# Kernel optimization log

Hardware: AMD Instinct MI355X
Metric: run time of the kernel (lower is better)

## Reference

```python
import jax, jax.numpy as jnp
import numpy as np

N_HEADS = 16
EMBED_DIM = 1024
HEAD_DIM = EMBED_DIM // N_HEADS
B, S = 4, 2048


def setup_inputs() -> dict:
    key = jax.random.key(0)
    k1, k2, k3, k4 = jax.random.split(key, 4)
    scale = 1.0 / np.sqrt(EMBED_DIM)
    x = jax.random.normal(k1, (B, S, EMBED_DIM), dtype=jnp.float32)
    Wq = jax.random.normal(k2, (EMBED_DIM, EMBED_DIM), dtype=jnp.float32) * scale
    Wk = jax.random.normal(k3, (EMBED_DIM, EMBED_DIM), dtype=jnp.float32) * scale
    Wv = jax.random.normal(k4, (EMBED_DIM, EMBED_DIM), dtype=jnp.float32) * scale
    return {"x": x, "Wq": Wq, "Wk": Wk, "Wv": Wv}


def reference(x, Wq, Wk, Wv):
    b, s, d = x.shape
    # torch nn.Linear(bias=False): y = x @ W.T
    def proj(W):
        return (x @ W.T).reshape(b, s, N_HEADS, HEAD_DIM).transpose(0, 2, 1, 3)  # [b,h,s,hd]
    q, k, v = proj(Wq), proj(Wk), proj(Wv)
    # scores scaled by sqrt(embed_dim) as in the source (not head_dim)
    scores = jnp.einsum('bhqd,bhkd->bhqk', q, k) / jnp.sqrt(jnp.float32(d))
    attn = jax.nn.softmax(scores, axis=-1)
    out = jnp.einsum('bhqk,bhkd->bhqd', attn, v)  # [b,h,s,hd]
    return out.transpose(0, 2, 1, 3).reshape(b, s, d)
```

## Files before the change

### kernel.cpp

```cpp
#include <hip/hip_runtime.h>

#define S_LEN  2048
#define NHEAD  16
#define HDIM   64
#define DMODEL 1024
#define XN     (4 * 2048 * 1024)
#define WN     (1024 * 1024)

typedef float  floatx4 __attribute__((ext_vector_type(4)));
typedef __bf16 bf16x8  __attribute__((ext_vector_type(8)));
typedef __bf16 bf16x4  __attribute__((ext_vector_type(4)));
typedef unsigned int u32;

union B8 {
  bf16x8 v8;
  bf16x4 v4[2];
  __bf16 e[8];
  uint4  u;
};

typedef __attribute__((address_space(1))) u32 gu32;
typedef __attribute__((address_space(3))) u32 lu32;
__device__ __forceinline__ void gld16(const void* g, void* l) {
  __builtin_amdgcn_global_load_lds((const gu32*)g, (lu32*)l, 16, 0, 0);
}

__global__ __launch_bounds__(256) void cvt_kernel(
    const float* __restrict__ x,  const float* __restrict__ Wq,
    const float* __restrict__ Wk, const float* __restrict__ Wv,
    __bf16* __restrict__ xb, __bf16* __restrict__ Wb)
{
  const size_t base = ((size_t)blockIdx.x * 256 + threadIdx.x) * 8;
  const float* src;
  __bf16* dst;
  float scl = 1.0f;
  if (base < XN) {
    src = x + base;
    dst = xb + base;
  } else {
    const size_t j = base - XN;
    const int mat = (int)(j >> 20);
    const size_t o = j & (WN - 1);
    src = (mat == 0 ? Wq : mat == 1 ? Wk : Wv) + o;
    dst = Wb + ((size_t)mat << 20) + o;
    if (mat == 0) scl = 0.045084220027780106f;
  }
  float4 a = *(const float4*)src;
  float4 b = *(const float4*)(src + 4);
  B8 r;
  r.e[0] = (__bf16)(a.x * scl); r.e[1] = (__bf16)(a.y * scl);
  r.e[2] = (__bf16)(a.z * scl); r.e[3] = (__bf16)(a.w * scl);
  r.e[4] = (__bf16)(b.x * scl); r.e[5] = (__bf16)(b.y * scl);
  r.e[6] = (__bf16)(b.z * scl); r.e[7] = (__bf16)(b.w * scl);
  *(bf16x8*)dst = r.v8;
}

__global__ __launch_bounds__(256) void proj_kernel(
    const __bf16* __restrict__ xb, const __bf16* __restrict__ Wb,
    __bf16* __restrict__ Qo, __bf16* __restrict__ Ko, __bf16* __restrict__ Vt)
{
  __shared__ __attribute__((aligned(16))) union {
    struct { __bf16 As[128 * 32]; __bf16 Bs[128 * 32]; } st;
    __bf16 Es[4][64][72];
  } sh;

  const int tid  = threadIdx.x;
  const int lane = tid & 63;
  const int wv   = tid >> 6;
  const int l15  = lane & 15;
  const int quad = lane >> 4;

  const int row0 = blockIdx.y * 128;
  const int n0   = blockIdx.x * 128;
  const int wrow = (wv >> 1) * 64;
  const int wcol = (wv & 1) * 64;

  floatx4 acc[4][4];
  #pragma unroll
  for (int i = 0; i < 4; i++)
    #pragma unroll
    for (int j = 0; j < 4; j++) acc[i][j] = (floatx4)0.0f;

  const int swz = quad ^ ((l15 >> 1) & 3);

  for (int kk = 0; kk < DMODEL; kk += 32) {
    #pragma unroll
    for (int i = 0; i < 2; i++) {
      const int c    = tid + i * 256;
      const int r    = c >> 2;
      const int glog = (c & 3) ^ ((c >> 3) & 3);
      const size_t lofs = (size_t)(wv * 64 + i * 256) * 8;
      gld16(xb + (size_t)(row0 + r) * DMODEL + kk + glog * 8, sh.st.As + lofs);
      gld16(Wb + (size_t)(n0 + r) * DMODEL + kk + glog * 8, sh.st.Bs + lofs);
    }
    __syncthreads();

    B8 af[4], bg[4];
    #pragma unroll
    for (int mb = 0; mb < 4; mb++)
      af[mb].u = *(const uint4*)(sh.st.As + (size_t)(wrow + mb * 16 + l15) * 32 + swz * 8);
    #pragma unroll
    for (int nb = 0; nb < 4; nb++)
      bg[nb].u = *(const uint4*)(sh.st.Bs + (size_t)(wcol + nb * 16 + l15) * 32 + swz * 8);

    #pragma unroll
    for (int mb = 0; mb < 4; mb++)
      #pragma unroll
      for (int nb = 0; nb < 4; nb++)
        acc[mb][nb] = __builtin_amdgcn_mfma_f32_16x16x32_bf16(
            af[mb].v8, bg[nb].v8, acc[mb][nb], 0, 0, 0);
    __syncthreads();
  }

  const int mat   = n0 >> 10;
  const int bb    = (row0 + wrow) >> 11;
  const int sbase = (row0 + wrow) & 2047;
  const int hh    = ((n0 & 1023) + wcol) >> 6;
  __syncthreads();

  if (mat < 2) {
    #pragma unroll
    for (int mb = 0; mb < 4; mb++)
      #pragma unroll
      for (int rr = 0; rr < 4; rr++)
        #pragma unroll
        for (int nb = 0; nb < 4; nb++)
          sh.Es[wv][mb * 16 + quad * 4 + rr][nb * 16 + l15] =
              (__bf16)acc[mb][nb][rr];
    __bf16* Out = (mat == 0) ? Qo : Ko;
    const size_t obase = ((size_t)(bb * NHEAD + hh) * S_LEN + sbase) * HDIM;
    #pragma unroll
    for (int t = 0; t < 8; t++) {
      const int lin = t * 64 + lane;
      const int s = lin >> 3, g = lin & 7;
      *(uint4*)&Out[obase + (size_t)s * HDIM + g * 8] =
          *(const uint4*)&sh.Es[wv][s][g * 8];
    }
  } else {
    #pragma unroll
    for (int mb = 0; mb < 4; mb++)
      #pragma unroll
      for (int nb = 0; nb < 4; nb++) {
        bf16x4 pk = { (__bf16)acc[mb][nb][0], (__bf16)acc[mb][nb][1],
                      (__bf16)acc[mb][nb][2], (__bf16)acc[mb][nb][3] };
        *(bf16x4*)&sh.Es[wv][nb * 16 + l15][mb * 16 + quad * 4] = pk;
      }
    const size_t vbase = (size_t)(bb * NHEAD + hh) * HDIM * S_LEN;
    #pragma unroll
    for (int t = 0; t < 8; t++) {
      const int lin = t * 64 + lane;
      const int d = lin >> 3, g = lin & 7;
      const u32 r0 = *(const u32*)&sh.Es[wv][d][2 * g];
      const u32 r1 = *(const u32*)&sh.Es[wv][d][16 + 2 * g];
      const u32 r2 = *(const u32*)&sh.Es[wv][d][32 + 2 * g];
      const u32 r3 = *(const u32*)&sh.Es[wv][d][48 + 2 * g];
      uint4 o;
      o.x = (r0 & 0xFFFFu) | (r1 << 16);
      o.y = (r2 & 0xFFFFu) | (r3 << 16);
      o.z = (r0 >> 16) | (r1 & 0xFFFF0000u);
      o.w = (r2 >> 16) | (r3 & 0xFFFF0000u);
      *(uint4*)&Vt[vbase + (size_t)d * S_LEN + sbase + g * 8] = o;
    }
  }
}

__global__ __launch_bounds__(256, 2) void attn_kernel(
    const __bf16* __restrict__ Q, const __bf16* __restrict__ K,
    const __bf16* __restrict__ Vt, float* __restrict__ out)
{
  __shared__ __attribute__((aligned(16))) __bf16 Ks[64 * 64];
  __shared__ __attribute__((aligned(16))) __bf16 Vs[64 * 64];
  __shared__ __attribute__((aligned(16))) __bf16 Pw[4][64][72];

  const int tid  = threadIdx.x;
  const int lane = tid & 63;
  const int wv   = tid >> 6;
  const int l15  = lane & 15;
  const int quad = lane >> 4;

  const int bh = blockIdx.y;
  const int q0 = blockIdx.x * 256;
  const int b  = bh >> 4;
  const int h  = bh & 15;

  const __bf16* Qb = Q  + (size_t)bh * S_LEN * HDIM;
  const __bf16* Kb = K  + (size_t)bh * S_LEN * HDIM;
  const __bf16* Vb = Vt + (size_t)bh * HDIM * S_LEN;

  B8 aq[4][2];
  #pragma unroll
  for (int mb = 0; mb < 4; mb++)
    #pragma unroll
    for (int kc = 0; kc < 2; kc++)
      aq[mb][kc].u = *(const uint4*)
          &Qb[(size_t)(q0 + wv * 64 + mb * 16 + l15) * HDIM + kc * 32 + quad * 8];

  floatx4 o[4][4];
  float rs[4][4];
  #pragma unroll
  for (int mb = 0; mb < 4; mb++) {
    #pragma unroll
    for (int nb = 0; nb < 4; nb++) o[mb][nb] = (floatx4)0.0f;
    #pragma unroll
    for (int r = 0; r < 4; r++) rs[mb][r] = 0.0f;
  }

  const int swz0 = quad ^ (l15 & 7);
  const int swz1 = (4 + quad) ^ (l15 & 7);

  for (int kv0 = 0; kv0 < S_LEN; kv0 += 64) {
    #pragma unroll
    for (int i = 0; i < 2; i++) {
      const int c    = tid + i * 256;
      const int r    = c >> 3;
      const int glog = (c & 7) ^ ((c >> 3) & 7);
      const size_t lofs = (size_t)(wv * 64 + i * 256) * 8;
      gld16(Kb + (size_t)(kv0 + r) * HDIM + glog * 8, Ks + lofs);
      gld16(Vb + (size_t)r * S_LEN + kv0 + glog * 8, Vs + lofs);
    }
    __syncthreads();

    floatx4 sa[4][4];
    #pragma unroll
    for (int mb = 0; mb < 4; mb++)
      #pragma unroll
      for (int nb = 0; nb < 4; nb++) sa[mb][nb] = (floatx4)0.0f;

    #pragma unroll
    for (int kc = 0; kc < 2; kc++) {
      const int sw = kc ? swz1 : swz0;
      B8 bk[4];
      #pragma unroll
      for (int nb = 0; nb < 4; nb++)
        bk[nb].u = *(const uint4*)(Ks + (size_t)(nb * 16 + l15) * 64 + sw * 8);
      #pragma unroll
      for (int mb = 0; mb < 4; mb++)
        #pragma unroll
        for (int nb = 0; nb < 4; nb++)
          sa[mb][nb] = __builtin_amdgcn_mfma_f32_16x16x32_bf16(
              aq[mb][kc].v8, bk[nb].v8, sa[mb][nb], 0, 0, 0);
    }

    #pragma unroll
    for (int mb = 0; mb < 4; mb++) {
      #pragma unroll
      for (int r = 0; r < 4; r++) {
        const float p0 = __builtin_amdgcn_exp2f(sa[mb][0][r]);
        const float p1 = __builtin_amdgcn_exp2f(sa[mb][1][r]);
        const float p2 = __builtin_amdgcn_exp2f(sa[mb][2][r]);
        const float p3 = __builtin_amdgcn_exp2f(sa[mb][3][r]);
        rs[mb][r] += (p0 + p1) + (p2 + p3);
        bf16x4 pk = { (__bf16)p0, (__bf16)p1, (__bf16)p2, (__bf16)p3 };
        *(bf16x4*)&Pw[wv][mb * 16 + quad * 4 + r][l15 * 4] = pk;
      }
    }

    #pragma unroll
    for (int kc = 0; kc < 2; kc++) {
      const int sw = kc ? swz1 : swz0;
      B8 ap[4], bv[4];
      #pragma unroll
      for (int mb = 0; mb < 4; mb++)
        ap[mb].u = *(const uint4*)&Pw[wv][mb * 16 + l15][kc * 32 + quad * 8];
      #pragma unroll
      for (int nb = 0; nb < 4; nb++)
        bv[nb].u = *(const uint4*)(Vs + (size_t)(nb * 16 + l15) * 64 + sw * 8);
      #pragma unroll
      for (int mb = 0; mb < 4; mb++)
        #pragma unroll
        for (int nb = 0; nb < 4; nb++)
          o[mb][nb] = __builtin_amdgcn_mfma_f32_16x16x32_bf16(
              ap[mb].v8, bv[nb].v8, o[mb][nb], 0, 0, 0);
    }
    __syncthreads();
  }

  #pragma unroll
  for (int mb = 0; mb < 4; mb++) {
    #pragma unroll
    for (int r = 0; r < 4; r++) {
      float v = rs[mb][r];
      v += __shfl_xor(v, 1);
      v += __shfl_xor(v, 2);
      v += __shfl_xor(v, 4);
      v += __shfl_xor(v, 8);
      const float inv  = 1.0f / v;
      const int   srow = q0 + wv * 64 + mb * 16 + quad * 4 + r;
      #pragma unroll
      for (int nb = 0; nb < 4; nb++) {
        out[((size_t)(b * S_LEN + srow)) * DMODEL + h * HDIM + nb * 16 + l15] =
            o[mb][nb][r] * inv;
      }
    }
  }
}

extern "C" void kernel_launch(void* const* d_in, const int* in_sizes, int n_in,
                              void* d_out, int out_size, void* d_ws, size_t ws_size,
                              hipStream_t stream) {
  const float* x  = (const float*)d_in[0];
  const float* Wq = (const float*)d_in[1];
  const float* Wk = (const float*)d_in[2];
  const float* Wv = (const float*)d_in[3];
  float* out = (float*)d_out;

  __bf16* xb = (__bf16*)d_ws;
  __bf16* Wb = xb + XN;
  __bf16* Q  = Wb + 3 * (size_t)WN;
  __bf16* K  = Q + (size_t)XN;
  __bf16* Vt = K + (size_t)XN;

  dim3 b256(256);
  cvt_kernel<<<dim3((XN + 3 * WN) / (256 * 8)), b256, 0, stream>>>(
      x, Wq, Wk, Wv, xb, Wb);

  dim3 g1(24, 64);
  proj_kernel<<<g1, b256, 0, stream>>>(xb, Wb, Q, K, Vt);

  dim3 g2(8, 64);
  attn_kernel<<<g2, b256, 0, stream>>>(Q, K, Vt, out);
}
```

Measured before the change: 225.0 us.

## Compute transposed attention scores so P stays in registers, skipping LDS round-trip

The attention kernel now computes S^T = K·Q^T and O^T = V^T·P^T. The exponentiated scores then sit directly in the MFMA B-operand layout, so the per-wave Pw shared buffer, its LDS writes and reads are gone. The projection kernel's V-transpose write is permuted so the stored Vt column order matches the new operand layout, which reduces that store to a plain 16-byte copy. Row sums now reduce across quads with fewer shuffles, output is written as float4, and the grid is swapped so blocks of the same head launch adjacently. The cost is more live registers for the exponent values, and correctness depends on the permuted Vt ordering matching the P fragment order.

```diff
diff --git a/kernel.cpp b/kernel.cpp
--- a/kernel.cpp
+++ b/kernel.cpp
@@ -143,23 +143,17 @@
       for (int nb = 0; nb < 4; nb++) {
         bf16x4 pk = { (__bf16)acc[mb][nb][0], (__bf16)acc[mb][nb][1],
                       (__bf16)acc[mb][nb][2], (__bf16)acc[mb][nb][3] };
-        *(bf16x4*)&sh.Es[wv][nb * 16 + l15][mb * 16 + quad * 4] = pk;
+        const int col = 32 * (mb >> 1) + 16 * (quad >> 1) + 8 * (quad & 1) +
+                        4 * (mb & 1);
+        *(bf16x4*)&sh.Es[wv][nb * 16 + l15][col] = pk;
       }
     const size_t vbase = (size_t)(bb * NHEAD + hh) * HDIM * S_LEN;
     #pragma unroll
     for (int t = 0; t < 8; t++) {
       const int lin = t * 64 + lane;
       const int d = lin >> 3, g = lin & 7;
-      const u32 r0 = *(const u32*)&sh.Es[wv][d][2 * g];
-      const u32 r1 = *(const u32*)&sh.Es[wv][d][16 + 2 * g];
-      const u32 r2 = *(const u32*)&sh.Es[wv][d][32 + 2 * g];
-      const u32 r3 = *(const u32*)&sh.Es[wv][d][48 + 2 * g];
-      uint4 o;
-      o.x = (r0 & 0xFFFFu) | (r1 << 16);
-      o.y = (r2 & 0xFFFFu) | (r3 << 16);
-      o.z = (r0 >> 16) | (r1 & 0xFFFF0000u);
-      o.w = (r2 >> 16) | (r3 & 0xFFFF0000u);
-      *(uint4*)&Vt[vbase + (size_t)d * S_LEN + sbase + g * 8] = o;
+      *(uint4*)&Vt[vbase + (size_t)d * S_LEN + sbase + g * 8] =
+          *(const uint4*)&sh.Es[wv][d][g * 8];
     }
   }
 }
@@ -170,7 +164,6 @@
 {
   __shared__ __attribute__((aligned(16))) __bf16 Ks[64 * 64];
   __shared__ __attribute__((aligned(16))) __bf16 Vs[64 * 64];
-  __shared__ __attribute__((aligned(16))) __bf16 Pw[4][64][72];
 
   const int tid  = threadIdx.x;
   const int lane = tid & 63;
@@ -178,8 +171,8 @@
   const int l15  = lane & 15;
   const int quad = lane >> 4;
 
-  const int bh = blockIdx.y;
-  const int q0 = blockIdx.x * 256;
+  const int bh = blockIdx.x;
+  const int q0 = blockIdx.y * 256;
   const int b  = bh >> 4;
   const int h  = bh & 15;
 
@@ -189,21 +182,20 @@
 
   B8 aq[4][2];
   #pragma unroll
-  for (int mb = 0; mb < 4; mb++)
+  for (int nb = 0; nb < 4; nb++)
     #pragma unroll
     for (int kc = 0; kc < 2; kc++)
-      aq[mb][kc].u = *(const uint4*)
-          &Qb[(size_t)(q0 + wv * 64 + mb * 16 + l15) * HDIM + kc * 32 + quad * 8];
+      aq[nb][kc].u = *(const uint4*)
+          &Qb[(size_t)(q0 + wv * 64 + nb * 16 + l15) * HDIM + kc * 32 + quad * 8];
 
   floatx4 o[4][4];
-  float rs[4][4];
-  #pragma unroll
-  for (int mb = 0; mb < 4; mb++) {
-    #pragma unroll
-    for (int nb = 0; nb < 4; nb++) o[mb][nb] = (floatx4)0.0f;
-    #pragma unroll
-    for (int r = 0; r < 4; r++) rs[mb][r] = 0.0f;
-  }
+  float rs[4];
+  #pragma unroll
+  for (int mt = 0; mt < 4; mt++)
+    #pragma unroll
+    for (int nb = 0; nb < 4; nb++) o[mt][nb] = (floatx4)0.0f;
+  #pragma unroll
+  for (int nb = 0; nb < 4; nb++) rs[nb] = 0.0f;
 
   const int swz0 = quad ^ (l15 & 7);
   const int swz1 = (4 + quad) ^ (l15 & 7);
@@ -222,75 +214,72 @@
 
     floatx4 sa[4][4];
     #pragma unroll
-    for (int mb = 0; mb < 4; mb++)
-      #pragma unroll
-      for (int nb = 0; nb < 4; nb++) sa[mb][nb] = (floatx4)0.0f;
+    for (int t = 0; t < 4; t++)
+      #pragma unroll
+      for (int nb = 0; nb < 4; nb++) sa[t][nb] = (floatx4)0.0f;
 
     #pragma unroll
     for (int kc = 0; kc < 2; kc++) {
       const int sw = kc ? swz1 : swz0;
-      B8 bk[4];
-      #pragma unroll
-      for (int nb = 0; nb < 4; nb++)
-        bk[nb].u = *(const uint4*)(Ks + (size_t)(nb * 16 + l15) * 64 + sw * 8);
-      #pragma unroll
-      for (int mb = 0; mb < 4; mb++)
+      B8 ak[4];
+      #pragma unroll
+      for (int t = 0; t < 4; t++)
+        ak[t].u = *(const uint4*)(Ks + (size_t)(t * 16 + l15) * 64 + sw * 8);
+      #pragma unroll
+      for (int t = 0; t < 4; t++)
         #pragma unroll
         for (int nb = 0; nb < 4; nb++)
-          sa[mb][nb] = __builtin_amdgcn_mfma_f32_16x16x32_bf16(
-              aq[mb][kc].v8, bk[nb].v8, sa[mb][nb], 0, 0, 0);
-    }
-
-    #pragma unroll
-    for (int mb = 0; mb < 4; mb++) {
-      #pragma unroll
-      for (int r = 0; r < 4; r++) {
-        const float p0 = __builtin_amdgcn_exp2f(sa[mb][0][r]);
-        const float p1 = __builtin_amdgcn_exp2f(sa[mb][1][r]);
-        const float p2 = __builtin_amdgcn_exp2f(sa[mb][2][r]);
-        const float p3 = __builtin_amdgcn_exp2f(sa[mb][3][r]);
-        rs[mb][r] += (p0 + p1) + (p2 + p3);
-        bf16x4 pk = { (__bf16)p0, (__bf16)p1, (__bf16)p2, (__bf16)p3 };
-        *(bf16x4*)&Pw[wv][mb * 16 + quad * 4 + r][l15 * 4] = pk;
-      }
+          sa[t][nb] = __builtin_amdgcn_mfma_f32_16x16x32_bf16(
+              ak[t].v8, aq[nb][kc].v8, sa[t][nb], 0, 0, 0);
     }
 
     #pragma unroll
     for (int kc = 0; kc < 2; kc++) {
       const int sw = kc ? swz1 : swz0;
-      B8 ap[4], bv[4];
-      #pragma unroll
-      for (int mb = 0; mb < 4; mb++)
-        ap[mb].u = *(const uint4*)&Pw[wv][mb * 16 + l15][kc * 32 + quad * 8];
-      #pragma unroll
-      for (int nb = 0; nb < 4; nb++)
-        bv[nb].u = *(const uint4*)(Vs + (size_t)(nb * 16 + l15) * 64 + sw * 8);
-      #pragma unroll
-      for (int mb = 0; mb < 4; mb++)
+      B8 pf[4];
+      #pragma unroll
+      for (int nb = 0; nb < 4; nb++) {
+        float e0 = __builtin_amdgcn_exp2f(sa[2 * kc][nb][0]);
+        float e1 = __builtin_amdgcn_exp2f(sa[2 * kc][nb][1]);
+        float e2 = __builtin_amdgcn_exp2f(sa[2 * kc][nb][2]);
+        float e3 = __builtin_amdgcn_exp2f(sa[2 * kc][nb][3]);
+        float e4 = __builtin_amdgcn_exp2f(sa[2 * kc + 1][nb][0]);
+        float e5 = __builtin_amdgcn_exp2f(sa[2 * kc + 1][nb][1]);
+        float e6 = __builtin_amdgcn_exp2f(sa[2 * kc + 1][nb][2]);
+        float e7 = __builtin_amdgcn_exp2f(sa[2 * kc + 1][nb][3]);
+        rs[nb] += ((e0 + e1) + (e2 + e3)) + ((e4 + e5) + (e6 + e7));
+        pf[nb].e[0] = (__bf16)e0; pf[nb].e[1] = (__bf16)e1;
+        pf[nb].e[2] = (__bf16)e2; pf[nb].e[3] = (__bf16)e3;
+        pf[nb].e[4] = (__bf16)e4; pf[nb].e[5] = (__bf16)e5;
+        pf[nb].e[6] = (__bf16)e6; pf[nb].e[7] = (__bf16)e7;
+      }
+      B8 av[4];
+      #pragma unroll
+      for (int mt = 0; mt < 4; mt++)
+        av[mt].u = *(const uint4*)(Vs + (size_t)(mt * 16 + l15) * 64 + sw * 8);
+      #pragma unroll
+      for (int mt = 0; mt < 4; mt++)
         #pragma unroll
         for (int nb = 0; nb < 4; nb++)
-          o[mb][nb] = __builtin_amdgcn_mfma_f32_16x16x32_bf16(
-              ap[mb].v8, bv[nb].v8, o[mb][nb], 0, 0, 0);
+          o[mt][nb] = __builtin_amdgcn_mfma_f32_16x16x32_bf16(
+              av[mt].v8, pf[nb].v8, o[mt][nb], 0, 0, 0);
     }
     __syncthreads();
   }
 
   #pragma unroll
-  for (int mb = 0; mb < 4; mb++) {
-    #pragma unroll
-    for (int r = 0; r < 4; r++) {
-      float v = rs[mb][r];
-      v += __shfl_xor(v, 1);
-      v += __shfl_xor(v, 2);
-      v += __shfl_xor(v, 4);
-      v += __shfl_xor(v, 8);
-      const float inv  = 1.0f / v;
-      const int   srow = q0 + wv * 64 + mb * 16 + quad * 4 + r;
-      #pragma unroll
-      for (int nb = 0; nb < 4; nb++) {
-        out[((size_t)(b * S_LEN + srow)) * DMODEL + h * HDIM + nb * 16 + l15] =
-            o[mb][nb][r] * inv;
-      }
+  for (int nb = 0; nb < 4; nb++) {
+    float v = rs[nb];
+    v += __shfl_xor(v, 16);
+    v += __shfl_xor(v, 32);
+    const float inv = 1.0f / v;
+    const int q = q0 + wv * 64 + nb * 16 + l15;
+    #pragma unroll
+    for (int mt = 0; mt < 4; mt++) {
+      float4 w = { o[mt][nb][0] * inv, o[mt][nb][1] * inv,
+                   o[mt][nb][2] * inv, o[mt][nb][3] * inv };
+      *(float4*)&out[((size_t)(b * S_LEN + q)) * DMODEL + h * HDIM +
+                     mt * 16 + quad * 4] = w;
     }
   }
 }
@@ -317,6 +306,6 @@
   dim3 g1(24, 64);
   proj_kernel<<<g1, b256, 0, stream>>>(xb, Wb, Q, K, Vt);
 
-  dim3 g2(8, 64);
+  dim3 g2(64, 8);
   attn_kernel<<<g2, b256, 0, stream>>>(Q, K, Vt, out);
 }
```

Result: faster. 218.2 us (-3.0%).
